# Kernel optimization log

Measured on AMD Instinct MI355X. Metric: run time of the kernel, lower is better.

Reference implementation:

```python
import jax, jax.numpy as jnp
import numpy as np

MAX_ITER = 10   # float32 branch of cg()
TOL = 1e-10

def _cdot(a, b):
    # complex_dot: sum(conj(a) * b) over all elements
    return jnp.sum(jnp.conj(a) * b)

def _A(p, smaps, mask):
    # p: [H,W] complex, smaps: [C,H,W] complex, mask: [H,W] real
    return jnp.fft.fft2(smaps * p[None], norm='ortho') * mask[None]

def _AH(y, smaps, mask):
    imgs = jnp.fft.ifft2(y * mask[None], norm='ortho')
    return jnp.sum(jnp.conj(smaps) * imgs, axis=0)  # [H,W]

def _cg(M, rhs):
    # conjugate gradient, faithful to the TF while_loop body
    def cond(s):
        i, rTr, x, r, p = s
        return jnp.logical_and(i < MAX_ITER, rTr > TOL)
    def body(s):
        i, rTr, x, r, p = s
        Ap = M(p)
        alpha = rTr / jnp.real(_cdot(p, Ap))
        x = x + p * alpha
        r = r - Ap * alpha
        rTrNew = jnp.real(_cdot(r, r))
        beta = rTrNew / rTr
        p = r + p * beta
        return (i + 1, rTrNew, x, r, p)
    rTr0 = jnp.real(_cdot(rhs, rhs))
    s0 = (jnp.int32(0), rTr0, jnp.zeros_like(rhs), rhs, rhs)
    return jax.lax.while_loop(cond, body, s0)[2]

def _solve_one(lambdaa, rhs, smaps, mask):
    M = lambda p: _AH(_A(p, smaps, mask), smaps, mask) + p * lambdaa
    return _cg(M, rhs)

_solve_b = jax.vmap(_solve_one, in_axes=(None, 0, 0, 0))  # replaces map_fn
_AH_b = jax.vmap(_AH, in_axes=(0, 0, 0))

def setup_inputs():
    key = jax.random.key(0)
    ks = jax.random.split(key, 7)
    B, C, H, W = 4, 16, 384, 384
    f = lambda k, s: jax.random.normal(k, s, dtype=jnp.float32)
    return {
        'lambdaa': 0.05 * jnp.ones((), jnp.float32),
        'x_re': f(ks[0], (B, H, W)),
        'x_im': f(ks[1], (B, H, W)),
        'y_re': f(ks[2], (B, C, H, W)),
        'y_im': f(ks[3], (B, C, H, W)),
        'smaps_re': f(ks[4], (B, C, H, W)),
        'smaps_im': f(ks[5], (B, C, H, W)),
        'mask': (jax.random.uniform(ks[6], (B, H, W)) < 0.33).astype(jnp.float32),
    }

def reference(lambdaa, x_re, x_im, y_re, y_im, smaps_re, smaps_im, mask):
    x = jax.lax.complex(x_re, x_im)
    y = jax.lax.complex(y_re, y_im)
    smaps = jax.lax.complex(smaps_re, smaps_im)
    # rhs = AH(y) + lambdaa * x
    rhs = _AH_b(y, smaps, mask) + x * lambdaa
    out = _solve_b(lambdaa, rhs, smaps, mask)  # [B,H,W] complex
    return jnp.stack([out.real, out.imag], axis=-1)  # [B,H,W,2] float32
```

## Files before the change

kernel.cpp:

```cpp
#include <hip/hip_runtime.h>


#define Bn 4
#define Cn 16
#define Hn 384
#define Wn 384
#define NPIX (Hn*Wn)
#define TPB 256
#define TOLF 1e-10f
#define NITER 10
#define RED_BLKS 72
#define GRP 4
#define CPG (Cn/GRP)
#define RPITCH 416
#define CPITCH 420

__device__ __forceinline__ float2 cadd(float2 a, float2 b){ return make_float2(a.x+b.x, a.y+b.y); }
__device__ __forceinline__ float2 csub(float2 a, float2 b){ return make_float2(a.x-b.x, a.y-b.y); }
__device__ __forceinline__ float2 cmulf(float2 a, float2 b){
  return make_float2(a.x*b.x - a.y*b.y, a.x*b.y + a.y*b.x);
}

__device__ __forceinline__ void wave_fence(){ asm volatile("s_waitcnt lgkmcnt(0)" ::: "memory"); }

template<int IMM>
__device__ __forceinline__ float2 shx(float2 v){
  int x = __builtin_amdgcn_ds_swizzle(__float_as_int(v.x), IMM);
  int y = __builtin_amdgcn_ds_swizzle(__float_as_int(v.y), IMM);
  return make_float2(__int_as_float(x), __int_as_float(y));
}

__device__ __forceinline__ int rev5(int x){
  return ((x&1)<<4) | ((x&2)<<2) | (x&4) | ((x&8)>>2) | ((x&16)>>4);
}

__device__ __forceinline__ int offmap(int w){ return w + ((w*683)>>13); }

template<int DIR>
__device__ __forceinline__ void fft12(float2* v)
{
  const float S3 = (DIR<0) ? -0.86602540378443864676f : 0.86602540378443864676f;
  const float sg = (DIR<0) ? -1.f : 1.f;
  float2 t[4][3];
#pragma unroll
  for (int b = 0; b < 4; ++b) {
    float2 a0 = v[b], a1 = v[4+b], a2 = v[8+b];
    float2 s = cadd(a1,a2), d = csub(a1,a2);
    float2 mm = make_float2(a0.x - 0.5f*s.x, a0.y - 0.5f*s.y);
    float2 e  = make_float2(-d.y*S3, d.x*S3);
    t[b][0] = cadd(a0,s);
    t[b][1] = cadd(mm,e);
    t[b][2] = csub(mm,e);
  }
  const float2 w1  = make_float2(0.86602540378443864676f, sg*0.5f);
  const float2 w2  = make_float2(0.5f, sg*0.86602540378443864676f);
  const float2 w3  = make_float2(0.f, sg);
  const float2 w4t = make_float2(-0.5f, sg*0.86602540378443864676f);
  const float2 w6  = make_float2(-1.f, 0.f);
  t[1][1] = cmulf(t[1][1], w1);  t[1][2] = cmulf(t[1][2], w2);
  t[2][1] = cmulf(t[2][1], w2);  t[2][2] = cmulf(t[2][2], w4t);
  t[3][1] = cmulf(t[3][1], w3);  t[3][2] = cmulf(t[3][2], w6);
#pragma unroll
  for (int c = 0; c < 3; ++c) {
    float2 e = cadd(t[0][c], t[2][c]);
    float2 f = csub(t[0][c], t[2][c]);
    float2 g = cadd(t[1][c], t[3][c]);
    float2 h = csub(t[1][c], t[3][c]);
    float2 ih = (DIR<0) ? make_float2(h.y, -h.x) : make_float2(-h.y, h.x);
    v[c]   = cadd(e,g);
    v[c+3] = cadd(f,ih);
    v[c+6] = csub(e,g);
    v[c+9] = csub(f,ih);
  }
}

template<int DIR>
__device__ __forceinline__ void fft32_lanes(float2* v, int li)
{
  const float c2pi = (DIR<0) ? -6.2831853071795864769f : 6.2831853071795864769f;
  const float sg   = (DIR<0) ? -1.f : 1.f;
  float s, c;
  __sincosf(c2pi*(1.f/32.f)*(float)(li&15), &s, &c); float2 wA = make_float2(c,s);
  __sincosf(c2pi*(1.f/16.f)*(float)(li&7),  &s, &c); float2 wB = make_float2(c,s);
  __sincosf(c2pi*(1.f/ 8.f)*(float)(li&3),  &s, &c); float2 wC = make_float2(c,s);
  bool bA = li & 16, bB = li & 8, bC = li & 4, bD = li & 2, bE = li & 1;
#pragma unroll
  for (int k = 0; k < 12; ++k) {
    float2 a = v[k], o;
    o = shx<0x401F>(a); a = bA ? cmulf(csub(o,a), wA) : cadd(a,o);
    o = shx<0x201F>(a); a = bB ? cmulf(csub(o,a), wB) : cadd(a,o);
    o = shx<0x101F>(a); a = bC ? cmulf(csub(o,a), wC) : cadd(a,o);
    o = shx<0x081F>(a);
    { float2 su = cadd(a,o), d = csub(o,a);
      float2 dw = bE ? make_float2(-sg*d.y, sg*d.x) : d;
      a = bD ? dw : su; }
    o = shx<0x041F>(a); a = bE ? csub(o,a) : cadd(a,o);
    v[k] = a;
  }
}

template<int DIR>
__device__ __forceinline__ void fft384(float2* v, int li)
{
  fft12<DIR>(v);
  const float c2pi = (DIR<0) ? -6.2831853071795864769f : 6.2831853071795864769f;
  float s, c;
  __sincosf(c2pi*(1.f/384.f)*(float)li, &s, &c);
  float2 W = make_float2(c,s), cw = W;
#pragma unroll
  for (int k = 1; k < 12; ++k) { v[k] = cmulf(v[k], cw); cw = cmulf(cw, W); }
  fft32_lanes<DIR>(v, li);
}


__global__ __launch_bounds__(TPB) void k_row_fwd(
    const float2* __restrict__ p, const float* __restrict__ Sre,
    const float* __restrict__ Sim, float2* __restrict__ tmp)
{
  __shared__ float2 lbuf[8*RPITCH];
  int tid = threadIdx.x;
  int wave = tid>>6, lane = tid&63, sub = lane>>5, li = lane&31;
  int row = wave*2 + sub;
  int tile = blockIdx.x % (Hn/8);
  int bc   = blockIdx.x / (Hn/8);
  int b = bc / Cn;
  int h = tile*8 + row;
  size_t gbase = (size_t)bc*NPIX + (size_t)h*Wn;
  size_t pbase = (size_t)b*NPIX + (size_t)h*Wn;

  float2 v[12];
#pragma unroll
  for (int k = 0; k < 12; ++k) {
    int w = 32*k + li;
    float2 pv = p[pbase + w];
    float sr = Sre[gbase + w], si = Sim[gbase + w];
    v[k] = make_float2(sr*pv.x - si*pv.y, sr*pv.y + si*pv.x);
  }
  fft384<-1>(v, li);
  int m = rev5(li);
  float2* lrow = lbuf + row*RPITCH;
#pragma unroll
  for (int k = 0; k < 12; ++k) lrow[13*m + k] = v[k];
  wave_fence();
#pragma unroll
  for (int k = 0; k < 12; ++k) {
    int w = 32*k + li;
    tmp[gbase + w] = lrow[offmap(w)];
  }
}

__global__ __launch_bounds__(TPB) void k_row_inv_acc(
    const float2* __restrict__ tmp, const float* __restrict__ Sre,
    const float* __restrict__ Sim, float2* __restrict__ partial)
{
  __shared__ float2 lbuf[8*RPITCH];
  int tid = threadIdx.x;
  int wave = tid>>6, lane = tid&63, sub = lane>>5, li = lane&31;
  int row = wave*2 + sub;
  int tile = blockIdx.x % (Hn/8);
  int rest = blockIdx.x / (Hn/8);
  int g = rest % GRP;
  int b = rest / GRP;
  int h = tile*8 + row;
  int m = rev5(li);
  float2* lrow = lbuf + row*RPITCH;

  float2 acc[12];
#pragma unroll
  for (int k = 0; k < 12; ++k) acc[k] = make_float2(0.f, 0.f);

  for (int j = 0; j < CPG; ++j) {
    size_t bc = (size_t)b*Cn + (g*CPG + j);
    size_t gbase = bc*NPIX + (size_t)h*Wn;
    float2 v[12];
#pragma unroll
    for (int k = 0; k < 12; ++k) v[k] = tmp[gbase + 32*k + li];
    fft384<1>(v, li);
    wave_fence();
#pragma unroll
    for (int k = 0; k < 12; ++k) lrow[13*m + k] = v[k];
    wave_fence();
#pragma unroll
    for (int k = 0; k < 12; ++k) {
      int w = 32*k + li;
      float2 u = lrow[offmap(w)];
      float sr = Sre[gbase + w], si = Sim[gbase + w];
      acc[k].x += sr*u.x + si*u.y;
      acc[k].y += sr*u.y - si*u.x;
    }
  }
  size_t pbase = ((size_t)g*Bn + b)*NPIX + (size_t)h*Wn;
#pragma unroll
  for (int k = 0; k < 12; ++k) partial[pbase + 32*k + li] = acc[k];
}

__global__ __launch_bounds__(TPB) void k_col_full(
    float2* __restrict__ tmp, const float* __restrict__ mask)
{
  __shared__ float2 dbuf[8*CPITCH];
  __shared__ float  mbuf[8*CPITCH];
  int tid = threadIdx.x;
  int wave = tid>>6, lane = tid&63, sub = lane>>5, li = lane&31;
  int col = wave*2 + sub;
  int tile = blockIdx.x % (Wn/8);
  int bc   = blockIdx.x / (Wn/8);
  int b = bc / Cn;
  int w0 = tile*8;
  size_t tbase = (size_t)bc*NPIX;
  size_t mbase = (size_t)b*NPIX;

  for (int e = tid; e < 8*Hn; e += TPB) {
    int wi = e & 7, h = e >> 3;
    int off = offmap(h);
    dbuf[wi*CPITCH + off] = tmp[tbase + (size_t)h*Wn + w0 + wi];
    mbuf[wi*CPITCH + off] = mask[mbase + (size_t)h*Wn + w0 + wi];
  }
  __syncthreads();

  float2* drow = dbuf + col*CPITCH;
  float*  mrow = mbuf + col*CPITCH;
  int m = rev5(li);
  float2 v[12];
#pragma unroll
  for (int k = 0; k < 12; ++k) v[k] = drow[offmap(32*k + li)];
  fft384<-1>(v, li);
  const float SC = 1.0f / (float)NPIX;
#pragma unroll
  for (int k = 0; k < 12; ++k) {
    float mv = mrow[13*m + k] * SC;
    v[k] = make_float2(v[k].x*mv, v[k].y*mv);
  }
  wave_fence();
#pragma unroll
  for (int k = 0; k < 12; ++k) drow[13*m + k] = v[k];
  wave_fence();
#pragma unroll
  for (int k = 0; k < 12; ++k) v[k] = drow[offmap(32*k + li)];
  fft384<1>(v, li);
  wave_fence();
#pragma unroll
  for (int k = 0; k < 12; ++k) drow[13*m + k] = v[k];
  __syncthreads();

  for (int e = tid; e < 8*Hn; e += TPB) {
    int wi = e & 7, h = e >> 3;
    tmp[tbase + (size_t)h*Wn + w0 + wi] = dbuf[wi*CPITCH + offmap(h)];
  }
}

__global__ __launch_bounds__(TPB) void k_col_rhs(
    const float* __restrict__ yre, const float* __restrict__ yim,
    const float* __restrict__ mask, float2* __restrict__ tmp)
{
  __shared__ float2 dbuf[8*CPITCH];
  int tid = threadIdx.x;
  int wave = tid>>6, lane = tid&63, sub = lane>>5, li = lane&31;
  int col = wave*2 + sub;
  int tile = blockIdx.x % (Wn/8);
  int bc   = blockIdx.x / (Wn/8);
  int b = bc / Cn;
  int w0 = tile*8;
  size_t tbase = (size_t)bc*NPIX;
  size_t mbase = (size_t)b*NPIX;

  for (int e = tid; e < 8*Hn; e += TPB) {
    int wi = e & 7, h = e >> 3;
    size_t gi = (size_t)h*Wn + w0 + wi;
    float mv = mask[mbase + gi] * (1.0f/384.0f);
    dbuf[wi*CPITCH + offmap(h)] = make_float2(yre[tbase+gi]*mv, yim[tbase+gi]*mv);
  }
  __syncthreads();

  float2* drow = dbuf + col*CPITCH;
  int m = rev5(li);
  float2 v[12];
#pragma unroll
  for (int k = 0; k < 12; ++k) v[k] = drow[offmap(32*k + li)];
  fft384<1>(v, li);
  wave_fence();
#pragma unroll
  for (int k = 0; k < 12; ++k) drow[13*m + k] = v[k];
  __syncthreads();

  for (int e = tid; e < 8*Hn; e += TPB) {
    int wi = e & 7, h = e >> 3;
    tmp[tbase + (size_t)h*Wn + w0 + wi] = dbuf[wi*CPITCH + offmap(h)];
  }
}


__global__ void k_zero_scal(float* __restrict__ scal)
{
  int i = threadIdx.x;
  if (i < 96) scal[i] = 0.0f;
}

__device__ __forceinline__ void block_reduce_atomic(float sum, float* target)
{
  __shared__ float red[TPB];
  red[threadIdx.x] = sum; __syncthreads();
  for (int s = TPB/2; s > 0; s >>= 1) {
    if (threadIdx.x < s) red[threadIdx.x] += red[threadIdx.x + s];
    __syncthreads();
  }
  if (threadIdx.x == 0) unsafeAtomicAdd(target, red[0]);
}

__global__ __launch_bounds__(TPB) void k_rhs_init(
    const float* __restrict__ xre, const float* __restrict__ xim,
    const float* __restrict__ lam, const float2* __restrict__ partial,
    float2* __restrict__ r, float2* __restrict__ p, float2* __restrict__ x,
    float* __restrict__ scal)
{
  int b = blockIdx.y;
  float l = lam[0];
  float sum = 0.0f;
  for (int i = blockIdx.x*TPB + threadIdx.x; i < NPIX; i += RED_BLKS*TPB) {
    size_t gi = (size_t)b*NPIX + i;
    float2 rv = make_float2(l*xre[gi], l*xim[gi]);
#pragma unroll
    for (int g = 0; g < GRP; ++g) {
      float2 pv = partial[((size_t)g*Bn + b)*NPIX + i];
      rv.x += pv.x; rv.y += pv.y;
    }
    r[gi] = rv; p[gi] = rv;
    x[gi] = make_float2(0.0f, 0.0f);
    sum += rv.x*rv.x + rv.y*rv.y;
  }
  block_reduce_atomic(sum, &scal[b]);
}

__global__ __launch_bounds__(TPB) void k_combine_dot(
    const float2* __restrict__ p, const float* __restrict__ lam,
    const float2* __restrict__ partial, float2* __restrict__ Ap,
    float* __restrict__ slot)
{
  int b = blockIdx.y;
  float l = lam[0];
  float sum = 0.0f;
  for (int i = blockIdx.x*TPB + threadIdx.x; i < NPIX; i += RED_BLKS*TPB) {
    size_t gi = (size_t)b*NPIX + i;
    float2 pv = p[gi];
    float2 av = make_float2(l*pv.x, l*pv.y);
#pragma unroll
    for (int g = 0; g < GRP; ++g) {
      float2 qv = partial[((size_t)g*Bn + b)*NPIX + i];
      av.x += qv.x; av.y += qv.y;
    }
    Ap[gi] = av;
    sum += pv.x*av.x + pv.y*av.y;
  }
  block_reduce_atomic(sum, &slot[b]);
}

__global__ __launch_bounds__(TPB) void k_upd1(
    float2* __restrict__ x, float2* __restrict__ r,
    const float2* __restrict__ p, const float2* __restrict__ Ap,
    const float* __restrict__ rtr_cur, float* __restrict__ rtr_new,
    const float* __restrict__ pap)
{
  int b = blockIdx.y;
  float rtr = rtr_cur[b];
  bool act = rtr > TOLF;
  float alpha = act ? rtr / pap[b] : 0.0f;
  float sum = 0.0f;
  for (int i = blockIdx.x*TPB + threadIdx.x; i < NPIX; i += RED_BLKS*TPB) {
    size_t gi = (size_t)b*NPIX + i;
    float2 rv = r[gi];
    if (act) {
      float2 pv = p[gi], av = Ap[gi], xv = x[gi];
      xv.x += alpha*pv.x; xv.y += alpha*pv.y;
      rv.x -= alpha*av.x; rv.y -= alpha*av.y;
      x[gi] = xv; r[gi] = rv;
    }
    sum += rv.x*rv.x + rv.y*rv.y;
  }
  block_reduce_atomic(sum, &rtr_new[b]);
}

__global__ __launch_bounds__(TPB) void k_upd2(
    float2* __restrict__ p, const float2* __restrict__ r,
    const float* __restrict__ rtr_cur, const float* __restrict__ rtr_new)
{
  int b = blockIdx.y;
  float rtr = rtr_cur[b];
  if (!(rtr > TOLF)) return;
  float beta = rtr_new[b] / rtr;
  for (int i = blockIdx.x*TPB + threadIdx.x; i < NPIX; i += RED_BLKS*TPB) {
    size_t gi = (size_t)b*NPIX + i;
    float2 rv = r[gi];
    float2 pv = p[gi];
    p[gi] = make_float2(rv.x + beta*pv.x, rv.y + beta*pv.y);
  }
}


extern "C" void kernel_launch(void* const* d_in, const int* in_sizes, int n_in,
                              void* d_out, int out_size, void* d_ws, size_t ws_size,
                              hipStream_t stream)
{
  const float* lam  = (const float*)d_in[0];
  const float* xre  = (const float*)d_in[1];
  const float* xim  = (const float*)d_in[2];
  const float* yre  = (const float*)d_in[3];
  const float* yim  = (const float*)d_in[4];
  const float* sre  = (const float*)d_in[5];
  const float* sim  = (const float*)d_in[6];
  const float* mask = (const float*)d_in[7];

  char* ws = (char*)d_ws;
  float2* tmp  = (float2*)ws;  ws += (size_t)Bn*Cn*NPIX*sizeof(float2);
  float2* part = (float2*)ws;  ws += (size_t)GRP*Bn*NPIX*sizeof(float2);
  float2* r    = (float2*)ws;  ws += (size_t)Bn*NPIX*sizeof(float2);
  float2* p    = (float2*)ws;  ws += (size_t)Bn*NPIX*sizeof(float2);
  float2* Ap   = (float2*)ws;  ws += (size_t)Bn*NPIX*sizeof(float2);
  float*  scal = (float*)ws;
  float2* x    = (float2*)d_out;

  dim3 blk(TPB);
  dim3 rg(RED_BLKS, Bn);
  int grid_row = Bn*Cn*(Hn/8);
  int grid_col = Bn*Cn*(Wn/8);
  int grid_inv = Bn*GRP*(Hn/8);

  k_zero_scal<<<1, 128, 0, stream>>>(scal);

  k_col_rhs<<<grid_col, blk, 0, stream>>>(yre, yim, mask, tmp);
  k_row_inv_acc<<<grid_inv, blk, 0, stream>>>(tmp, sre, sim, part);
  k_rhs_init<<<rg, blk, 0, stream>>>(xre, xim, lam, part, r, p, x, scal);

  for (int it = 0; it < NITER; ++it) {
    k_row_fwd<<<grid_row, blk, 0, stream>>>(p, sre, sim, tmp);
    k_col_full<<<grid_col, blk, 0, stream>>>(tmp, mask);
    k_row_inv_acc<<<grid_inv, blk, 0, stream>>>(tmp, sre, sim, part);
    k_combine_dot<<<rg, blk, 0, stream>>>(p, lam, part, Ap, scal + 44 + it*Bn);
    k_upd1<<<rg, blk, 0, stream>>>(x, r, p, Ap, scal + it*Bn, scal + (it+1)*Bn, scal + 44 + it*Bn);
    if (it < NITER-1)
      k_upd2<<<rg, blk, 0, stream>>>(p, r, scal + it*Bn, scal + (it+1)*Bn);
  }
}
```

Before: 1.622 ms.

## Widen column FFT tiles, precompute permuted mask, use more coil groups

Column FFT kernels now process 16 columns per 512-thread block with a tighter LDS pitch. The per-block mask staging through shared memory is replaced by a one-time precomputed mask, laid out in the FFT's bit-reversed order and prescaled, which each lane reads with three float4 loads. When the workspace is large enough, the coil reduction in the inverse row pass is split into 8 groups of 2 coils instead of 4 groups of 4, raising parallelism at the cost of more partial-sum traffic in the combine kernels. The larger LDS footprint per block may reduce occupancy, and the mask kernel adds a launch.

```diff
diff --git a/kernel.cpp b/kernel.cpp
--- a/kernel.cpp
+++ b/kernel.cpp
@@ -7,13 +7,13 @@
 #define Wn 384
 #define NPIX (Hn*Wn)
 #define TPB 256
+#define CTPB 512
+#define NCOL 16
 #define TOLF 1e-10f
 #define NITER 10
 #define RED_BLKS 72
-#define GRP 4
-#define CPG (Cn/GRP)
 #define RPITCH 416
-#define CPITCH 420
+#define CPITCH 417
 
 __device__ __forceinline__ float2 cadd(float2 a, float2 b){ return make_float2(a.x+b.x, a.y+b.y); }
 __device__ __forceinline__ float2 csub(float2 a, float2 b){ return make_float2(a.x-b.x, a.y-b.y); }
@@ -149,18 +149,20 @@
   }
 }
 
+template<int CPGt>
 __global__ __launch_bounds__(TPB) void k_row_inv_acc(
     const float2* __restrict__ tmp, const float* __restrict__ Sre,
     const float* __restrict__ Sim, float2* __restrict__ partial)
 {
+  const int GRPt = Cn/CPGt;
   __shared__ float2 lbuf[8*RPITCH];
   int tid = threadIdx.x;
   int wave = tid>>6, lane = tid&63, sub = lane>>5, li = lane&31;
   int row = wave*2 + sub;
   int tile = blockIdx.x % (Hn/8);
   int rest = blockIdx.x / (Hn/8);
-  int g = rest % GRP;
-  int b = rest / GRP;
+  int g = rest % GRPt;
+  int b = rest / GRPt;
   int h = tile*8 + row;
   int m = rev5(li);
   float2* lrow = lbuf + row*RPITCH;
@@ -169,8 +171,8 @@
 #pragma unroll
   for (int k = 0; k < 12; ++k) acc[k] = make_float2(0.f, 0.f);
 
-  for (int j = 0; j < CPG; ++j) {
-    size_t bc = (size_t)b*Cn + (g*CPG + j);
+  for (int j = 0; j < CPGt; ++j) {
+    size_t bc = (size_t)b*Cn + (g*CPGt + j);
     size_t gbase = bc*NPIX + (size_t)h*Wn;
     float2 v[12];
 #pragma unroll
@@ -194,42 +196,48 @@
   for (int k = 0; k < 12; ++k) partial[pbase + 32*k + li] = acc[k];
 }
 
-__global__ __launch_bounds__(TPB) void k_col_full(
-    float2* __restrict__ tmp, const float* __restrict__ mask)
-{
-  __shared__ float2 dbuf[8*CPITCH];
-  __shared__ float  mbuf[8*CPITCH];
+__global__ __launch_bounds__(TPB) void k_maskp(
+    const float* __restrict__ mask, float* __restrict__ maskP)
+{
+  int idx = blockIdx.x*TPB + threadIdx.x;
+  if (idx >= Bn*NPIX) return;
+  int k = idx % 12; int t = idx / 12;
+  int li = t & 31; t >>= 5;
+  int w = t % Wn;  int b = t / Wn;
+  maskP[idx] = mask[((size_t)b*Hn + (k + 12*rev5(li)))*Wn + w] * (1.0f/(float)NPIX);
+}
+
+__global__ __launch_bounds__(CTPB) void k_col_full(
+    float2* __restrict__ tmp, const float* __restrict__ maskP)
+{
+  __shared__ float2 dbuf[NCOL*CPITCH];
   int tid = threadIdx.x;
   int wave = tid>>6, lane = tid&63, sub = lane>>5, li = lane&31;
   int col = wave*2 + sub;
-  int tile = blockIdx.x % (Wn/8);
-  int bc   = blockIdx.x / (Wn/8);
+  int tile = blockIdx.x % (Wn/NCOL);
+  int bc   = blockIdx.x / (Wn/NCOL);
   int b = bc / Cn;
-  int w0 = tile*8;
+  int w0 = tile*NCOL;
   size_t tbase = (size_t)bc*NPIX;
-  size_t mbase = (size_t)b*NPIX;
-
-  for (int e = tid; e < 8*Hn; e += TPB) {
-    int wi = e & 7, h = e >> 3;
-    int off = offmap(h);
-    dbuf[wi*CPITCH + off] = tmp[tbase + (size_t)h*Wn + w0 + wi];
-    mbuf[wi*CPITCH + off] = mask[mbase + (size_t)h*Wn + w0 + wi];
+
+  for (int e = tid; e < NCOL*Hn; e += CTPB) {
+    int wi = e & (NCOL-1), h = e >> 4;
+    dbuf[wi*CPITCH + offmap(h)] = tmp[tbase + (size_t)h*Wn + w0 + wi];
   }
   __syncthreads();
 
   float2* drow = dbuf + col*CPITCH;
-  float*  mrow = mbuf + col*CPITCH;
+  int w = w0 + col;
   int m = rev5(li);
   float2 v[12];
 #pragma unroll
   for (int k = 0; k < 12; ++k) v[k] = drow[offmap(32*k + li)];
   fft384<-1>(v, li);
-  const float SC = 1.0f / (float)NPIX;
-#pragma unroll
-  for (int k = 0; k < 12; ++k) {
-    float mv = mrow[13*m + k] * SC;
-    v[k] = make_float2(v[k].x*mv, v[k].y*mv);
-  }
+  const float4* mp4 = (const float4*)(maskP + (((size_t)b*Wn + w)*32 + li)*12);
+  float4 m0 = mp4[0], m1 = mp4[1], m2 = mp4[2];
+  float mk[12] = {m0.x,m0.y,m0.z,m0.w, m1.x,m1.y,m1.z,m1.w, m2.x,m2.y,m2.z,m2.w};
+#pragma unroll
+  for (int k = 0; k < 12; ++k) v[k] = make_float2(v[k].x*mk[k], v[k].y*mk[k]);
   wave_fence();
 #pragma unroll
   for (int k = 0; k < 12; ++k) drow[13*m + k] = v[k];
@@ -242,29 +250,29 @@
   for (int k = 0; k < 12; ++k) drow[13*m + k] = v[k];
   __syncthreads();
 
-  for (int e = tid; e < 8*Hn; e += TPB) {
-    int wi = e & 7, h = e >> 3;
+  for (int e = tid; e < NCOL*Hn; e += CTPB) {
+    int wi = e & (NCOL-1), h = e >> 4;
     tmp[tbase + (size_t)h*Wn + w0 + wi] = dbuf[wi*CPITCH + offmap(h)];
   }
 }
 
-__global__ __launch_bounds__(TPB) void k_col_rhs(
+__global__ __launch_bounds__(CTPB) void k_col_rhs(
     const float* __restrict__ yre, const float* __restrict__ yim,
     const float* __restrict__ mask, float2* __restrict__ tmp)
 {
-  __shared__ float2 dbuf[8*CPITCH];
+  __shared__ float2 dbuf[NCOL*CPITCH];
   int tid = threadIdx.x;
   int wave = tid>>6, lane = tid&63, sub = lane>>5, li = lane&31;
   int col = wave*2 + sub;
-  int tile = blockIdx.x % (Wn/8);
-  int bc   = blockIdx.x / (Wn/8);
+  int tile = blockIdx.x % (Wn/NCOL);
+  int bc   = blockIdx.x / (Wn/NCOL);
   int b = bc / Cn;
-  int w0 = tile*8;
+  int w0 = tile*NCOL;
   size_t tbase = (size_t)bc*NPIX;
   size_t mbase = (size_t)b*NPIX;
 
-  for (int e = tid; e < 8*Hn; e += TPB) {
-    int wi = e & 7, h = e >> 3;
+  for (int e = tid; e < NCOL*Hn; e += CTPB) {
+    int wi = e & (NCOL-1), h = e >> 4;
     size_t gi = (size_t)h*Wn + w0 + wi;
     float mv = mask[mbase + gi] * (1.0f/384.0f);
     dbuf[wi*CPITCH + offmap(h)] = make_float2(yre[tbase+gi]*mv, yim[tbase+gi]*mv);
@@ -282,8 +290,8 @@
   for (int k = 0; k < 12; ++k) drow[13*m + k] = v[k];
   __syncthreads();
 
-  for (int e = tid; e < 8*Hn; e += TPB) {
-    int wi = e & 7, h = e >> 3;
+  for (int e = tid; e < NCOL*Hn; e += CTPB) {
+    int wi = e & (NCOL-1), h = e >> 4;
     tmp[tbase + (size_t)h*Wn + w0 + wi] = dbuf[wi*CPITCH + offmap(h)];
   }
 }
@@ -306,6 +314,7 @@
   if (threadIdx.x == 0) unsafeAtomicAdd(target, red[0]);
 }
 
+template<int GRPt>
 __global__ __launch_bounds__(TPB) void k_rhs_init(
     const float* __restrict__ xre, const float* __restrict__ xim,
     const float* __restrict__ lam, const float2* __restrict__ partial,
@@ -319,7 +328,7 @@
     size_t gi = (size_t)b*NPIX + i;
     float2 rv = make_float2(l*xre[gi], l*xim[gi]);
 #pragma unroll
-    for (int g = 0; g < GRP; ++g) {
+    for (int g = 0; g < GRPt; ++g) {
       float2 pv = partial[((size_t)g*Bn + b)*NPIX + i];
       rv.x += pv.x; rv.y += pv.y;
     }
@@ -330,6 +339,7 @@
   block_reduce_atomic(sum, &scal[b]);
 }
 
+template<int GRPt>
 __global__ __launch_bounds__(TPB) void k_combine_dot(
     const float2* __restrict__ p, const float* __restrict__ lam,
     const float2* __restrict__ partial, float2* __restrict__ Ap,
@@ -343,7 +353,7 @@
     float2 pv = p[gi];
     float2 av = make_float2(l*pv.x, l*pv.y);
 #pragma unroll
-    for (int g = 0; g < GRP; ++g) {
+    for (int g = 0; g < GRPt; ++g) {
       float2 qv = partial[((size_t)g*Bn + b)*NPIX + i];
       av.x += qv.x; av.y += qv.y;
     }
@@ -408,32 +418,50 @@
   const float* sim  = (const float*)d_in[6];
   const float* mask = (const float*)d_in[7];
 
+  const size_t szTmp  = (size_t)Bn*Cn*NPIX*sizeof(float2);
+  const size_t szVec  = (size_t)Bn*NPIX*sizeof(float2);
+  const size_t szMask = (size_t)Bn*NPIX*sizeof(float);
+  const size_t need8  = szTmp + 8*szVec + 3*szVec + 512 + szMask;
+  const int GRP = (ws_size >= need8) ? 8 : 4;
+
   char* ws = (char*)d_ws;
-  float2* tmp  = (float2*)ws;  ws += (size_t)Bn*Cn*NPIX*sizeof(float2);
-  float2* part = (float2*)ws;  ws += (size_t)GRP*Bn*NPIX*sizeof(float2);
-  float2* r    = (float2*)ws;  ws += (size_t)Bn*NPIX*sizeof(float2);
-  float2* p    = (float2*)ws;  ws += (size_t)Bn*NPIX*sizeof(float2);
-  float2* Ap   = (float2*)ws;  ws += (size_t)Bn*NPIX*sizeof(float2);
-  float*  scal = (float*)ws;
+  float2* tmp  = (float2*)ws;  ws += szTmp;
+  float2* part = (float2*)ws;  ws += (size_t)GRP*szVec;
+  float2* r    = (float2*)ws;  ws += szVec;
+  float2* p    = (float2*)ws;  ws += szVec;
+  float2* Ap   = (float2*)ws;  ws += szVec;
+  float*  scal = (float*)ws;   ws += 512;
+  float*  mskP = (float*)ws;
   float2* x    = (float2*)d_out;
 
   dim3 blk(TPB);
   dim3 rg(RED_BLKS, Bn);
   int grid_row = Bn*Cn*(Hn/8);
-  int grid_col = Bn*Cn*(Wn/8);
+  int grid_col = Bn*Cn*(Wn/NCOL);
   int grid_inv = Bn*GRP*(Hn/8);
 
   k_zero_scal<<<1, 128, 0, stream>>>(scal);
-
-  k_col_rhs<<<grid_col, blk, 0, stream>>>(yre, yim, mask, tmp);
-  k_row_inv_acc<<<grid_inv, blk, 0, stream>>>(tmp, sre, sim, part);
-  k_rhs_init<<<rg, blk, 0, stream>>>(xre, xim, lam, part, r, p, x, scal);
+  k_maskp<<<(Bn*NPIX + TPB-1)/TPB, blk, 0, stream>>>(mask, mskP);
+
+  k_col_rhs<<<grid_col, CTPB, 0, stream>>>(yre, yim, mask, tmp);
+  if (GRP == 8) {
+    k_row_inv_acc<2><<<grid_inv, blk, 0, stream>>>(tmp, sre, sim, part);
+    k_rhs_init<8><<<rg, blk, 0, stream>>>(xre, xim, lam, part, r, p, x, scal);
+  } else {
+    k_row_inv_acc<4><<<grid_inv, blk, 0, stream>>>(tmp, sre, sim, part);
+    k_rhs_init<4><<<rg, blk, 0, stream>>>(xre, xim, lam, part, r, p, x, scal);
+  }
 
   for (int it = 0; it < NITER; ++it) {
     k_row_fwd<<<grid_row, blk, 0, stream>>>(p, sre, sim, tmp);
-    k_col_full<<<grid_col, blk, 0, stream>>>(tmp, mask);
-    k_row_inv_acc<<<grid_inv, blk, 0, stream>>>(tmp, sre, sim, part);
-    k_combine_dot<<<rg, blk, 0, stream>>>(p, lam, part, Ap, scal + 44 + it*Bn);
+    k_col_full<<<grid_col, CTPB, 0, stream>>>(tmp, mskP);
+    if (GRP == 8) {
+      k_row_inv_acc<2><<<grid_inv, blk, 0, stream>>>(tmp, sre, sim, part);
+      k_combine_dot<8><<<rg, blk, 0, stream>>>(p, lam, part, Ap, scal + 44 + it*Bn);
+    } else {
+      k_row_inv_acc<4><<<grid_inv, blk, 0, stream>>>(tmp, sre, sim, part);
+      k_combine_dot<4><<<rg, blk, 0, stream>>>(p, lam, part, Ap, scal + 44 + it*Bn);
+    }
     k_upd1<<<rg, blk, 0, stream>>>(x, r, p, Ap, scal + it*Bn, scal + (it+1)*Bn, scal + 44 + it*Bn);
     if (it < NITER-1)
       k_upd2<<<rg, blk, 0, stream>>>(p, r, scal + it*Bn, scal + (it+1)*Bn);
```

Result: no change. 1.635 ms (+0.8%).
